# Performance work log

Measured on AMD Instinct MI355X. Metric: run time of the kernel, lower is better.

Reference implementation:

```python
import jax, jax.numpy as jnp
import numpy as np

UNITS = 1024
IN_DIM = 1024
BATCH = 4096


def setup_inputs() -> dict:
    key = jax.random.key(0)
    ks = jax.random.split(key, 11)
    C = UNITS + IN_DIM  # concat dim
    glorot = lambda k, shp: jax.random.uniform(k, shp, jnp.float32, -1.0, 1.0) * np.sqrt(6.0 / (shp[0] + shp[1]))
    return {
        "inputs": jax.random.normal(ks[0], (BATCH, IN_DIM), jnp.float32),
        "hidden_state": jax.random.normal(ks[1], (BATCH, UNITS), jnp.float32),
        "cell_state": jax.random.normal(ks[2], (BATCH, UNITS), jnp.float32),
        "W_f": glorot(ks[3], (C, UNITS)), "b_f": jnp.ones((UNITS,), jnp.float32),  # forget bias init = ones
        "W_i": glorot(ks[4], (C, UNITS)), "b_i": jnp.zeros((UNITS,), jnp.float32),
        "W_c": glorot(ks[5], (C, UNITS)), "b_c": jnp.zeros((UNITS,), jnp.float32),
        "W_o": glorot(ks[6], (C, UNITS)), "b_o": jnp.zeros((UNITS,), jnp.float32),
    }


def reference(inputs, hidden_state, cell_state, W_f, b_f, W_i, b_i, W_c, b_c, W_o, b_o):
    # concat order matches original: (hidden_state, inputs)
    x = jnp.concatenate((hidden_state, inputs), axis=1)  # [B, U+D]
    f = jax.nn.sigmoid(x @ W_f + b_f)
    i = jax.nn.sigmoid(x @ W_i + b_i)
    c_cand = jnp.tanh(x @ W_c + b_c)
    new_cell = f * cell_state + i * c_cand
    o = jax.nn.sigmoid(x @ W_o + b_o)
    new_hidden = o * jnp.tanh(new_cell)
    return (new_hidden, new_cell)
```

## Files before the change

kernel.cpp:

```cpp
#include <hip/hip_runtime.h>
#include <hip/hip_bf16.h>

#define BATCH  4096
#define UNITS  1024
#define CDIM   2048
#define NDIM   4096

typedef __attribute__((ext_vector_type(8))) short bf16x8;
typedef __attribute__((ext_vector_type(4))) float f32x4;

__device__ __forceinline__ void gload_lds16(const void* g, void* l) {
    __builtin_amdgcn_global_load_lds(
        (const __attribute__((address_space(1))) unsigned int*)g,
        (__attribute__((address_space(3))) unsigned int*)l, 16, 0, 0);
}

__device__ __forceinline__ float sigm(float x) { return 1.f / (1.f + __expf(-x)); }
__device__ __forceinline__ float tanh_fast(float x) { return 2.f / (1.f + __expf(-2.f * x)) - 1.f; }

__global__ void prep(const float* __restrict__ h, const float* __restrict__ in,
                     const float* __restrict__ Wf, const float* __restrict__ Wi,
                     const float* __restrict__ Wc, const float* __restrict__ Wo,
                     __hip_bfloat16* __restrict__ x, __hip_bfloat16* __restrict__ Wt) {
    __shared__ float tile[64 * 65];
    int b = blockIdx.x, tid = threadIdx.x;
    if (b < 4096) {
        int t   = b * 256 + tid;
        int row = t >> 8;
        int c8  = (t & 255) * 8;
        const float* src = (c8 < UNITS) ? (h + (size_t)row * UNITS + c8)
                                        : (in + (size_t)row * UNITS + (c8 - UNITS));
        float4 v0 = *(const float4*)src;
        float4 v1 = *(const float4*)(src + 4);
        union { __hip_bfloat16 b[8]; bf16x8 v; } pk;
        pk.b[0] = __float2bfloat16(v0.x); pk.b[1] = __float2bfloat16(v0.y);
        pk.b[2] = __float2bfloat16(v0.z); pk.b[3] = __float2bfloat16(v0.w);
        pk.b[4] = __float2bfloat16(v1.x); pk.b[5] = __float2bfloat16(v1.y);
        pk.b[6] = __float2bfloat16(v1.z); pk.b[7] = __float2bfloat16(v1.w);
        *(bf16x8*)(x + (size_t)row * CDIM + c8) = pk.v;
    } else {
        int idx = b - 4096;
        int g = idx >> 9, rest = idx & 511, ky = rest >> 4, ux = rest & 15;
        const float* W = (g == 0) ? Wf : (g == 1) ? Wi : (g == 2) ? Wc : Wo;
        int k0 = ky * 64, u0 = ux * 64;
#pragma unroll
        for (int q = 0; q < 4; ++q) {
            int s = q * 256 + tid;
            int row = s >> 4, c4 = s & 15;
            float4 v = *(const float4*)&W[(size_t)(k0 + row) * UNITS + u0 + c4 * 4];
            *(float4*)&tile[row * 65 + c4 * 4] = v;
        }
        __syncthreads();
#pragma unroll
        for (int q = 0; q < 2; ++q) {
            int s = q * 256 + tid;
            int u = s >> 3, kc = s & 7;
            int U = u0 + u;
            int n = ((U >> 5) << 7) + (((U >> 4) & 1) << 6) + (g << 4) + (U & 15);
            union { __hip_bfloat16 b[8]; bf16x8 v; } pk;
#pragma unroll
            for (int j = 0; j < 8; ++j)
                pk.b[j] = __float2bfloat16(tile[(kc * 8 + j) * 65 + u]);
            *(bf16x8*)(Wt + (size_t)n * CDIM + k0 + kc * 8) = pk.v;
        }
    }
}

__global__ __launch_bounds__(256, 2) void gemm_lstm(
    const __hip_bfloat16* __restrict__ A,
    const __hip_bfloat16* __restrict__ Bt,
    const float* __restrict__ b_f, const float* __restrict__ b_i,
    const float* __restrict__ b_c, const float* __restrict__ b_o,
    const float* __restrict__ cell,
    float* __restrict__ out)
{
    __shared__ short As[3][128 * 64];
    const int K = CDIM;

    int bid = blockIdx.x;
    int nb  = (bid & 7) * 2 + ((bid >> 3) & 1);
    int mb  = bid >> 4;
    int m0  = mb * 128, n0 = nb * 256;

    int tid  = threadIdx.x;
    int w    = tid >> 6, lane = tid & 63;
    int quad = lane >> 4, r16 = lane & 15;
    int wn   = w * 64;

    f32x4 acc[8][4];
#pragma unroll
    for (int i = 0; i < 8; ++i)
#pragma unroll
        for (int j = 0; j < 4; ++j) acc[i][j] = (f32x4){0.f, 0.f, 0.f, 0.f};

    const short* Ag = (const short*)A  + (size_t)m0 * K;
    const short* Bg = (const short*)Bt + (size_t)(n0 + wn + r16) * K + quad * 8;

    auto stageA = [&](short* dst, int k0) {
#pragma unroll
        for (int q = 0; q < 4; ++q) {
            int s    = q * 256 + tid;
            int row  = s >> 3;
            int cg   = (s & 7) ^ (row & 7);
            int lofs = (q * 256 + w * 64) * 8;
            gload_lds16(Ag + (size_t)row * K + k0 + cg * 8, dst + lofs);
        }
    };
    auto loadB = [&](bf16x8* dst, int k0) {
#pragma unroll
        for (int ks = 0; ks < 2; ++ks)
#pragma unroll
            for (int j = 0; j < 4; ++j)
                dst[ks * 4 + j] = *(const bf16x8*)&Bg[(size_t)(j * 16) * K + k0 + ks * 32];
    };
    auto compute = [&](const short* pA, const bf16x8* B) {
#pragma unroll
        for (int ks = 0; ks < 2; ++ks) {
            bf16x8 af[8];
            int kc = ((quad + ks * 4) ^ (r16 & 7)) * 8;
#pragma unroll
            for (int i = 0; i < 8; ++i)
                af[i] = *(const bf16x8*)&pA[(i * 16 + r16) * 64 + kc];
#pragma unroll
            for (int i = 0; i < 8; ++i)
#pragma unroll
                for (int j = 0; j < 4; ++j)
                    acc[i][j] = __builtin_amdgcn_mfma_f32_16x16x32_bf16(af[i], B[ks * 4 + j], acc[i][j], 0, 0, 0);
        }
    };

    short *p0 = As[0], *p1 = As[1], *p2 = As[2];
    bf16x8 B0[8], B1[8];
    stageA(p0, 0);
    stageA(p1, 64);
    loadB(B0, 0);

    for (int kt = 0; kt < K / 64; kt += 2) {
        asm volatile("s_waitcnt vmcnt(12)" ::: "memory");
        asm volatile("s_barrier" ::: "memory");
        stageA(p2, min((kt + 2) * 64, K - 64));
        loadB(B1, min((kt + 1) * 64, K - 64));
        compute(p0, B0);
        { short* t = p0; p0 = p1; p1 = p2; p2 = t; }

        asm volatile("s_waitcnt vmcnt(12)" ::: "memory");
        asm volatile("s_barrier" ::: "memory");
        stageA(p2, min((kt + 3) * 64, K - 64));
        loadB(B0, min((kt + 2) * 64, K - 64));
        compute(p0, B1);
        { short* t = p0; p0 = p1; p1 = p2; p2 = t; }
    }

    int u = nb * 64 + (w >> 1) * 32 + (w & 1) * 16 + r16;
    float bfv = b_f[u], biv = b_i[u], bcv = b_c[u], bov = b_o[u];
    float* out_h = out;
    float* out_c = out + (size_t)BATCH * UNITS;
#pragma unroll
    for (int i = 0; i < 8; ++i) {
#pragma unroll
        for (int rr = 0; rr < 4; ++rr) {
            int m = m0 + i * 16 + quad * 4 + rr;
            float fg = sigm(acc[i][0][rr] + bfv);
            float ig = sigm(acc[i][1][rr] + biv);
            float cc = tanh_fast(acc[i][2][rr] + bcv);
            float og = sigm(acc[i][3][rr] + bov);
            float cold = cell[(size_t)m * UNITS + u];
            float cn = fg * cold + ig * cc;
            out_h[(size_t)m * UNITS + u] = og * tanh_fast(cn);
            out_c[(size_t)m * UNITS + u] = cn;
        }
    }
}

extern "C" void kernel_launch(void* const* d_in, const int* in_sizes, int n_in,
                              void* d_out, int out_size, void* d_ws, size_t ws_size,
                              hipStream_t stream) {
    const float* inputs = (const float*)d_in[0];
    const float* hidden = (const float*)d_in[1];
    const float* cell   = (const float*)d_in[2];
    const float* Wf = (const float*)d_in[3];
    const float* bf_ = (const float*)d_in[4];
    const float* Wi = (const float*)d_in[5];
    const float* bi_ = (const float*)d_in[6];
    const float* Wc = (const float*)d_in[7];
    const float* bc_ = (const float*)d_in[8];
    const float* Wo = (const float*)d_in[9];
    const float* bo_ = (const float*)d_in[10];
    float* out = (float*)d_out;

    char* ws = (char*)d_ws;
    __hip_bfloat16* x  = (__hip_bfloat16*)ws;
    __hip_bfloat16* Wt = (__hip_bfloat16*)(ws + (16u << 20));

    prep<<<dim3(6144), dim3(256), 0, stream>>>(hidden, inputs, Wf, Wi, Wc, Wo, x, Wt);
    gemm_lstm<<<dim3(512), dim3(256), 0, stream>>>(
        x, Wt, bf_, bi_, bc_, bo_, cell, out);
}
```

Measured before the change: 220.3 us.

## Retile LSTM GEMM to 256x128 blocks with per-wave private A staging

Result: slower. 281.6 us (+27.8%).

```diff
diff --git a/kernel.cpp b/kernel.cpp
--- a/kernel.cpp
+++ b/kernel.cpp
@@ -56,7 +56,7 @@
             int s = q * 256 + tid;
             int u = s >> 3, kc = s & 7;
             int U = u0 + u;
-            int n = ((U >> 5) << 7) + (((U >> 4) & 1) << 6) + (g << 4) + (U & 15);
+            int n = ((U >> 5) << 7) + (g << 5) + (U & 31);
             union { __hip_bfloat16 b[8]; bf16x8 v; } pk;
 #pragma unroll
             for (int j = 0; j < 8; ++j)
@@ -74,100 +74,96 @@
     const float* __restrict__ cell,
     float* __restrict__ out)
 {
-    __shared__ short As[3][128 * 64];
+    __shared__ short As[4][2][64 * 32];
     const int K = CDIM;
 
     int bid = blockIdx.x;
-    int nb  = (bid & 7) * 2 + ((bid >> 3) & 1);
-    int mb  = bid >> 4;
-    int m0  = mb * 128, n0 = nb * 256;
+    int nb  = (bid & 7) * 4 + ((bid >> 3) & 3);
+    int mb  = bid >> 5;
+    int m0  = mb * 256, n0 = nb * 128;
 
     int tid  = threadIdx.x;
     int w    = tid >> 6, lane = tid & 63;
     int quad = lane >> 4, r16 = lane & 15;
-    int wn   = w * 64;
 
-    f32x4 acc[8][4];
+    f32x4 acc[4][8];
 #pragma unroll
-    for (int i = 0; i < 8; ++i)
+    for (int i = 0; i < 4; ++i)
 #pragma unroll
-        for (int j = 0; j < 4; ++j) acc[i][j] = (f32x4){0.f, 0.f, 0.f, 0.f};
+        for (int j = 0; j < 8; ++j) acc[i][j] = (f32x4){0.f, 0.f, 0.f, 0.f};
 
-    const short* Ag = (const short*)A  + (size_t)m0 * K;
-    const short* Bg = (const short*)Bt + (size_t)(n0 + wn + r16) * K + quad * 8;
+    const short* Ag = (const short*)A  + (size_t)(m0 + w * 64) * K;
+    const short* Bg = (const short*)Bt + (size_t)(n0 + r16) * K + quad * 8;
 
-    auto stageA = [&](short* dst, int k0) {
+    auto stage = [&](int p, int k0) {
+        short* dst = As[w][p];
 #pragma unroll
         for (int q = 0; q < 4; ++q) {
-            int s    = q * 256 + tid;
-            int row  = s >> 3;
-            int cg   = (s & 7) ^ (row & 7);
-            int lofs = (q * 256 + w * 64) * 8;
-            gload_lds16(Ag + (size_t)row * K + k0 + cg * 8, dst + lofs);
+            int s   = q * 64 + lane;
+            int row = s >> 2;
+            int cg  = (s & 3) ^ ((row >> 1) & 3);
+            gload_lds16(Ag + (size_t)row * K + k0 + cg * 8, dst + s * 8);
         }
     };
-    auto loadB = [&](bf16x8* dst, int k0) {
+    auto loadB = [&](bf16x8* Bv, int k0) {
 #pragma unroll
-        for (int ks = 0; ks < 2; ++ks)
+        for (int j = 0; j < 8; ++j)
+            Bv[j] = *(const bf16x8*)&Bg[(size_t)(j * 16) * K + k0];
+    };
+    auto compute = [&](int p, const bf16x8* Bv) {
+        bf16x8 af[4];
 #pragma unroll
-            for (int j = 0; j < 4; ++j)
-                dst[ks * 4 + j] = *(const bf16x8*)&Bg[(size_t)(j * 16) * K + k0 + ks * 32];
-    };
-    auto compute = [&](const short* pA, const bf16x8* B) {
+        for (int i = 0; i < 4; ++i) {
+            int row = i * 16 + r16;
+            int cs  = quad ^ ((r16 >> 1) & 3);
+            af[i] = *(const bf16x8*)&As[w][p][(row * 4 + cs) * 8];
+        }
 #pragma unroll
-        for (int ks = 0; ks < 2; ++ks) {
-            bf16x8 af[8];
-            int kc = ((quad + ks * 4) ^ (r16 & 7)) * 8;
+        for (int i = 0; i < 4; ++i)
 #pragma unroll
-            for (int i = 0; i < 8; ++i)
-                af[i] = *(const bf16x8*)&pA[(i * 16 + r16) * 64 + kc];
-#pragma unroll
-            for (int i = 0; i < 8; ++i)
-#pragma unroll
-                for (int j = 0; j < 4; ++j)
-                    acc[i][j] = __builtin_amdgcn_mfma_f32_16x16x32_bf16(af[i], B[ks * 4 + j], acc[i][j], 0, 0, 0);
-        }
+            for (int j = 0; j < 8; ++j)
+                acc[i][j] = __builtin_amdgcn_mfma_f32_16x16x32_bf16(af[i], Bv[j], acc[i][j], 0, 0, 0);
     };
 
-    short *p0 = As[0], *p1 = As[1], *p2 = As[2];
     bf16x8 B0[8], B1[8];
-    stageA(p0, 0);
-    stageA(p1, 64);
+    stage(0, 0);
     loadB(B0, 0);
 
-    for (int kt = 0; kt < K / 64; kt += 2) {
+    for (int kt = 0; kt < K / 32; kt += 2) {
+        int k1 = (kt + 1) * 32;
+        int k2 = min((kt + 2) * 32, K - 32);
+        stage(1, k1);
+        loadB(B1, k1);
         asm volatile("s_waitcnt vmcnt(12)" ::: "memory");
-        asm volatile("s_barrier" ::: "memory");
-        stageA(p2, min((kt + 2) * 64, K - 64));
-        loadB(B1, min((kt + 1) * 64, K - 64));
-        compute(p0, B0);
-        { short* t = p0; p0 = p1; p1 = p2; p2 = t; }
-
+        compute(0, B0);
+        asm volatile("" ::: "memory");
+        stage(0, k2);
+        loadB(B0, k2);
         asm volatile("s_waitcnt vmcnt(12)" ::: "memory");
-        asm volatile("s_barrier" ::: "memory");
-        stageA(p2, min((kt + 3) * 64, K - 64));
-        loadB(B0, min((kt + 2) * 64, K - 64));
-        compute(p0, B1);
-        { short* t = p0; p0 = p1; p1 = p2; p2 = t; }
+        compute(1, B1);
+        asm volatile("" ::: "memory");
     }
 
-    int u = nb * 64 + (w >> 1) * 32 + (w & 1) * 16 + r16;
-    float bfv = b_f[u], biv = b_i[u], bcv = b_c[u], bov = b_o[u];
     float* out_h = out;
     float* out_c = out + (size_t)BATCH * UNITS;
 #pragma unroll
-    for (int i = 0; i < 8; ++i) {
+    for (int uu = 0; uu < 2; ++uu) {
+        int u = nb * 32 + uu * 16 + r16;
+        float bfv = b_f[u], biv = b_i[u], bcv = b_c[u], bov = b_o[u];
 #pragma unroll
-        for (int rr = 0; rr < 4; ++rr) {
-            int m = m0 + i * 16 + quad * 4 + rr;
-            float fg = sigm(acc[i][0][rr] + bfv);
-            float ig = sigm(acc[i][1][rr] + biv);
-            float cc = tanh_fast(acc[i][2][rr] + bcv);
-            float og = sigm(acc[i][3][rr] + bov);
-            float cold = cell[(size_t)m * UNITS + u];
-            float cn = fg * cold + ig * cc;
-            out_h[(size_t)m * UNITS + u] = og * tanh_fast(cn);
-            out_c[(size_t)m * UNITS + u] = cn;
+        for (int i = 0; i < 4; ++i) {
+#pragma unroll
+            for (int rr = 0; rr < 4; ++rr) {
+                int m = m0 + w * 64 + i * 16 + quad * 4 + rr;
+                float fg = sigm(acc[i][0 * 2 + uu][rr] + bfv);
+                float ig = sigm(acc[i][1 * 2 + uu][rr] + biv);
+                float cc = tanh_fast(acc[i][2 * 2 + uu][rr] + bcv);
+                float og = sigm(acc[i][3 * 2 + uu][rr] + bov);
+                float cold = cell[(size_t)m * UNITS + u];
+                float cn = fg * cold + ig * cc;
+                out_h[(size_t)m * UNITS + u] = og * tanh_fast(cn);
+                out_c[(size_t)m * UNITS + u] = cn;
+            }
         }
     }
 }
```
